# Kernel optimization log

Measured on AMD Instinct MI355X. Metric: run time of the kernel, lower is better.

Reference implementation:

```python
import jax, jax.numpy as jnp
import numpy as np

B, T, H, OUT = 128, 1024, 256, 2


def setup_inputs() -> dict:
    key = jax.random.key(0)
    ks = jax.random.split(key, 16)
    s_in = 1.0 / np.sqrt(1 + H)
    s_2h = 1.0 / np.sqrt(2 * H)
    s_o = 1.0 / np.sqrt(H)
    return {
        "x": jax.random.normal(ks[0], (B, T, 2), dtype=jnp.float32),
        "h_0": jax.random.normal(ks[1], (1, B, H), dtype=jnp.float32) * 0.1,
        "Wa": jax.random.normal(ks[2], (1 + H, H), dtype=jnp.float32) * s_in,
        "ba": jnp.zeros((H,), dtype=jnp.float32),
        "Wp1": jax.random.normal(ks[3], (1 + H, H), dtype=jnp.float32) * s_in,
        "bp1": jnp.zeros((H,), dtype=jnp.float32),
        "Wp2": jax.random.normal(ks[4], (1 + H, H), dtype=jnp.float32) * s_in,
        "bp2": jnp.zeros((H,), dtype=jnp.float32),
        "Wz": jax.random.normal(ks[5], (2 * H, H), dtype=jnp.float32) * s_2h,
        "bz": jnp.zeros((H,), dtype=jnp.float32),
        "Wh": jax.random.normal(ks[6], (2 * H, H), dtype=jnp.float32) * s_2h,
        "bh": jnp.zeros((H,), dtype=jnp.float32),
        "Wo": jax.random.normal(ks[7], (H, OUT), dtype=jnp.float32) * s_o,
        "bo": jnp.zeros((OUT,), dtype=jnp.float32),
    }


def _pgjanet_scan(x, h0, Wa, ba, Wp1, bp1, Wp2, bp2, Wz, bz, Wh, bh):
    # x: [B, T, 2], h0: [B, H]
    xt_all = jnp.swapaxes(x, 0, 1)  # [T, B, 2]

    def step(h, xt):
        amp = xt[:, 0:1]                       # [B, 1]
        ph = xt[:, 1:2]                        # [B, 1]
        a = jnp.tanh(jnp.concatenate([amp, h], axis=-1) @ Wa + ba)
        p1 = jnp.tanh(jnp.concatenate([jnp.cos(ph), h], axis=-1) @ Wp1 + bp1)
        p2 = jnp.tanh(jnp.concatenate([jnp.sin(ph), h], axis=-1) @ Wp2 + bp2)
        u = a * p1 * p2 * (1 - a) * (1 - p1) * (1 - p2)
        newin = jnp.concatenate([u, h], axis=-1)  # [B, 2H]
        z = jax.nn.sigmoid(newin @ Wz + bz)
        h_cand = jnp.tanh(newin @ Wh + bh)
        h_new = z * h + (1 - z) * h_cand
        return h_new, h_new

    h_n, hs = jax.lax.scan(step, h0, xt_all)
    return jnp.swapaxes(hs, 0, 1), h_n  # [B, T, H], [B, H]


def reference(x, h_0, Wa, ba, Wp1, bp1, Wp2, bp2, Wz, bz, Wh, bh, Wo, bo):
    hs, h_n = _pgjanet_scan(x, h_0[0], Wa, ba, Wp1, bp1, Wp2, bp2, Wz, bz, Wh, bh)
    out = hs @ Wo + bo  # [B, T, OUT]
    return (out, h_n)
```

## Files before the change

kernel.cpp:

```cpp
#include <hip/hip_runtime.h>
#include <math.h>


#define B_   128
#define T_   1024
#define H_   256
#define GB   16
#define GC   16
#define MB   8
#define NS   16
#define NTHR 512
#define HPAD 264

typedef float    f32x4 __attribute__((ext_vector_type(4)));
typedef unsigned u32x4 __attribute__((ext_vector_type(4)));

__device__ __forceinline__ void sys_st_x4(unsigned* p, u32x4 v) {
  asm volatile("global_store_dwordx4 %0, %1, off sc0 sc1" :: "v"(p), "v"(v) : "memory");
}
__device__ __forceinline__ void sys_ld2_x4(const unsigned* p0, const unsigned* p1,
                                           u32x4& a, u32x4& b) {
  asm volatile("global_load_dwordx4 %0, %2, off sc0 sc1\n\t"
               "global_load_dwordx4 %1, %3, off sc0 sc1\n\t"
               "s_waitcnt vmcnt(0)"
               : "=&v"(a), "=&v"(b) : "v"(p0), "v"(p1) : "memory");
}

__launch_bounds__(NTHR, 1)
__global__ void pgjanet_persist(
    const float* __restrict__ x,   const float* __restrict__ h0,
    const float* __restrict__ Wa,  const float* __restrict__ ba,
    const float* __restrict__ Wp1, const float* __restrict__ bp1,
    const float* __restrict__ Wp2, const float* __restrict__ bp2,
    const float* __restrict__ Wz,  const float* __restrict__ bz,
    const float* __restrict__ Wh,  const float* __restrict__ bh,
    const float* __restrict__ Wo,  const float* __restrict__ bo,
    float* __restrict__ out,
    unsigned* __restrict__ u_ex,
    unsigned* __restrict__ h_ex)
{
  __shared__ __align__(16) float w1t[3 * NS * 256];
  __shared__ __align__(16) float w2t[2 * NS * 512];
  __shared__ __align__(16) float h_lds[MB * HPAD];
  __shared__ __align__(16) float u_lds[MB * HPAD];
  __shared__ __align__(16) float wo_s[H_ * 2];
  __shared__ __align__(16) float xin[2 * MB * 4];

  const int wg   = blockIdx.x;
  const int g    = wg >> 4;
  const int gc   = wg & (GC - 1);
  const int tid  = threadIdx.x;
  const int lane = tid & 63;
  const int wave = tid >> 6;
  const int mb   = lane >> 3;
  const int ks   = lane & 7;
  const int b0   = g * MB;
  const int n0   = gc * NS + wave * 2;

  for (int i = tid; i < 3 * NS * 256; i += NTHR) {
    int c = i >> 8, k = i & 255;
    int mat = c >> 4, n = c & 15;
    const float* W = (mat == 0) ? Wa : (mat == 1 ? Wp1 : Wp2);
    w1t[i] = W[(1 + k) * H_ + gc * NS + n];
  }
  for (int i = tid; i < 2 * NS * 512; i += NTHR) {
    int c = i >> 9, k = i & 511;
    int mat = c >> 4, n = c & 15;
    const float* W = (mat == 0) ? Wz : Wh;
    w2t[i] = W[k * H_ + gc * NS + n];
  }
  for (int i = tid; i < H_ * 2; i += NTHR) wo_s[i] = Wo[i];

  float w1r0_[6], b1_[6];
#pragma unroll
  for (int m = 0; m < 3; ++m) {
    const float* W  = (m == 0) ? Wa : (m == 1 ? Wp1 : Wp2);
    const float* bb = (m == 0) ? ba : (m == 1 ? bp1 : bp2);
#pragma unroll
    for (int cc = 0; cc < 2; ++cc) {
      w1r0_[m * 2 + cc] = W[n0 + cc];
      b1_[m * 2 + cc]   = bb[n0 + cc];
    }
  }
  float bz_[2] = { bz[n0], bz[n0 + 1] };
  float bh_[2] = { bh[n0], bh[n0 + 1] };
  const float bo0 = bo[0], bo1 = bo[1];

  {
    int flat = tid * 4;
    int mbb = flat >> 8, kk = flat & 255;
    *(f32x4*)(h_lds + mbb * HPAD + kk) = *(const f32x4*)(h0 + (b0 + mbb) * H_ + kk);
  }
  if (tid < MB) {
    float2 xt = *(const float2*)(x + ((b0 + tid) * T_) * 2);
    f32x4 xi; xi[0] = xt.x; xi[1] = cosf(xt.y); xi[2] = sinf(xt.y); xi[3] = 0.f;
    *(f32x4*)(xin + tid * 4) = xi;
  }
  __syncthreads();

  unsigned* u_exg = u_ex + g * 4096;
  unsigned* h_exg = h_ex + g * 4096;
  unsigned* u_my  = u_exg + ((gc * 8 + wave) * 8) * 4;
  unsigned* h_my  = h_exg + ((gc * 8 + wave) * 8) * 4;

  for (int t = 0; t < T_; ++t) {
    const unsigned seq = (unsigned)(t + 1);

    f32x4 hv[8];
#pragma unroll
    for (int kt = 0; kt < 8; ++kt)
      hv[kt] = *(const f32x4*)(h_lds + mb * HPAD + kt * 32 + ks * 4);

    float acc[6] = {0.f, 0.f, 0.f, 0.f, 0.f, 0.f};
#pragma unroll
    for (int kt = 0; kt < 8; ++kt) {
      f32x4 h4 = hv[kt];
#pragma unroll
      for (int m = 0; m < 3; ++m)
#pragma unroll
        for (int cc = 0; cc < 2; ++cc) {
          f32x4 w4 = *(const f32x4*)(w1t + (m * NS + wave * 2 + cc) * 256 + kt * 32 + ks * 4);
          float s = acc[m * 2 + cc];
          s = fmaf(h4[0], w4[0], s); s = fmaf(h4[1], w4[1], s);
          s = fmaf(h4[2], w4[2], s); s = fmaf(h4[3], w4[3], s);
          acc[m * 2 + cc] = s;
        }
    }
#pragma unroll
    for (int i = 0; i < 6; ++i) {
      float v = acc[i];
      v += __shfl_xor(v, 1);
      v += __shfl_xor(v, 2);
      v += __shfl_xor(v, 4);
      acc[i] = v;
    }
    if (ks == 0) {
      f32x4 xi = *(const f32x4*)(xin + ((t & 1) * MB + mb) * 4);
      float uu[2];
#pragma unroll
      for (int cc = 0; cc < 2; ++cc) {
        float a  = tanhf(acc[0 + cc] + xi[0] * w1r0_[0 + cc] + b1_[0 + cc]);
        float p1 = tanhf(acc[2 + cc] + xi[1] * w1r0_[2 + cc] + b1_[2 + cc]);
        float p2 = tanhf(acc[4 + cc] + xi[2] * w1r0_[4 + cc] + b1_[4 + cc]);
        uu[cc] = a * p1 * p2 * (1.f - a) * (1.f - p1) * (1.f - p2);
      }
      u32x4 ch;
      ch.x = __float_as_uint(uu[0]); ch.y = __float_as_uint(uu[1]);
      ch.z = seq; ch.w = 0u;
      sys_st_x4(u_my + mb * 4, ch);
    }

    if (t + 1 < T_ && tid < MB) {
      float2 xt = *(const float2*)(x + ((b0 + tid) * T_ + (t + 1)) * 2);
      f32x4 xi; xi[0] = xt.x; xi[1] = cosf(xt.y); xi[2] = sinf(xt.y); xi[3] = 0.f;
      *(f32x4*)(xin + (((t + 1) & 1) * MB + tid) * 4) = xi;
    }
    if (t > 0 && ((t - 1) & 15) == gc) {
      f32x4 h4  = *(const f32x4*)(h_lds + wave * HPAD + lane * 4);
      f32x4 wo0 = *(const f32x4*)(wo_s + lane * 8);
      f32x4 wo1 = *(const f32x4*)(wo_s + lane * 8 + 4);
      float v0 = h4[0] * wo0[0] + h4[1] * wo0[2] + h4[2] * wo1[0] + h4[3] * wo1[2];
      float v1 = h4[0] * wo0[1] + h4[1] * wo0[3] + h4[2] * wo1[1] + h4[3] * wo1[3];
      v0 += __shfl_xor(v0, 1);  v1 += __shfl_xor(v1, 1);
      v0 += __shfl_xor(v0, 2);  v1 += __shfl_xor(v1, 2);
      v0 += __shfl_xor(v0, 4);  v1 += __shfl_xor(v1, 4);
      v0 += __shfl_xor(v0, 8);  v1 += __shfl_xor(v1, 8);
      v0 += __shfl_xor(v0, 16); v1 += __shfl_xor(v1, 16);
      v0 += __shfl_xor(v0, 32); v1 += __shfl_xor(v1, 32);
      if (lane == 0) {
        float2 o; o.x = v0 + bo0; o.y = v1 + bo1;
        *(float2*)(out + ((b0 + wave) * T_ + (t - 1)) * 2) = o;
      }
    }
    float acc2[4] = {0.f, 0.f, 0.f, 0.f};
#pragma unroll
    for (int kt = 0; kt < 8; ++kt) {
      f32x4 h4 = hv[kt];
#pragma unroll
      for (int m = 0; m < 2; ++m)
#pragma unroll
        for (int cc = 0; cc < 2; ++cc) {
          f32x4 w4 = *(const f32x4*)(w2t + (m * NS + wave * 2 + cc) * 512 + 256 + kt * 32 + ks * 4);
          float s = acc2[m * 2 + cc];
          s = fmaf(h4[0], w4[0], s); s = fmaf(h4[1], w4[1], s);
          s = fmaf(h4[2], w4[2], s); s = fmaf(h4[3], w4[3], s);
          acc2[m * 2 + cc] = s;
        }
    }

    {
      u32x4 A, B;
      const unsigned* p0 = u_exg + tid * 4;
      const unsigned* p1 = u_exg + (tid + 512) * 4;
      for (;;) {
        sys_ld2_x4(p0, p1, A, B);
        if (A.z == seq && B.z == seq) break;
        __builtin_amdgcn_s_sleep(1);
      }
      int c = tid;
      float2 d0; d0.x = __uint_as_float(A.x); d0.y = __uint_as_float(A.y);
      *(float2*)(u_lds + (c & 7) * HPAD + (c >> 6) * 16 + ((c >> 3) & 7) * 2) = d0;
      c = tid + 512;
      float2 d1; d1.x = __uint_as_float(B.x); d1.y = __uint_as_float(B.y);
      *(float2*)(u_lds + (c & 7) * HPAD + (c >> 6) * 16 + ((c >> 3) & 7) * 2) = d1;
    }
    __syncthreads();

#pragma unroll
    for (int kt = 0; kt < 8; ++kt) {
      f32x4 u4 = *(const f32x4*)(u_lds + mb * HPAD + kt * 32 + ks * 4);
#pragma unroll
      for (int m = 0; m < 2; ++m)
#pragma unroll
        for (int cc = 0; cc < 2; ++cc) {
          f32x4 w4 = *(const f32x4*)(w2t + (m * NS + wave * 2 + cc) * 512 + kt * 32 + ks * 4);
          float s = acc2[m * 2 + cc];
          s = fmaf(u4[0], w4[0], s); s = fmaf(u4[1], w4[1], s);
          s = fmaf(u4[2], w4[2], s); s = fmaf(u4[3], w4[3], s);
          acc2[m * 2 + cc] = s;
        }
    }
#pragma unroll
    for (int i = 0; i < 4; ++i) {
      float v = acc2[i];
      v += __shfl_xor(v, 1);
      v += __shfl_xor(v, 2);
      v += __shfl_xor(v, 4);
      acc2[i] = v;
    }
    if (ks == 0) {
      float z0  = 1.f / (1.f + expf(-(acc2[0] + bz_[0])));
      float z1  = 1.f / (1.f + expf(-(acc2[1] + bz_[1])));
      float hc0 = tanhf(acc2[2] + bh_[0]);
      float hc1 = tanhf(acc2[3] + bh_[1]);
      float2 hp = *(const float2*)(h_lds + mb * HPAD + n0);
      float hn0 = z0 * hp.x + (1.f - z0) * hc0;
      float hn1 = z1 * hp.y + (1.f - z1) * hc1;
      u32x4 ch;
      ch.x = __float_as_uint(hn0); ch.y = __float_as_uint(hn1);
      ch.z = seq; ch.w = 0u;
      sys_st_x4(h_my + mb * 4, ch);
      if (t == T_ - 1) {
        float2 o; o.x = hn0; o.y = hn1;
        *(float2*)(out + B_ * T_ * 2 + (b0 + mb) * H_ + n0) = o;
      }
    }
    __syncthreads();

    {
      u32x4 A, B;
      const unsigned* p0 = h_exg + tid * 4;
      const unsigned* p1 = h_exg + (tid + 512) * 4;
      for (;;) {
        sys_ld2_x4(p0, p1, A, B);
        if (A.z == seq && B.z == seq) break;
        __builtin_amdgcn_s_sleep(1);
      }
      int c = tid;
      float2 d0; d0.x = __uint_as_float(A.x); d0.y = __uint_as_float(A.y);
      *(float2*)(h_lds + (c & 7) * HPAD + (c >> 6) * 16 + ((c >> 3) & 7) * 2) = d0;
      c = tid + 512;
      float2 d1; d1.x = __uint_as_float(B.x); d1.y = __uint_as_float(B.y);
      *(float2*)(h_lds + (c & 7) * HPAD + (c >> 6) * 16 + ((c >> 3) & 7) * 2) = d1;
    }
    __syncthreads();
  }

  if (gc == ((T_ - 1) & 15)) {
    f32x4 h4  = *(const f32x4*)(h_lds + wave * HPAD + lane * 4);
    f32x4 wo0 = *(const f32x4*)(wo_s + lane * 8);
    f32x4 wo1 = *(const f32x4*)(wo_s + lane * 8 + 4);
    float v0 = h4[0] * wo0[0] + h4[1] * wo0[2] + h4[2] * wo1[0] + h4[3] * wo1[2];
    float v1 = h4[0] * wo0[1] + h4[1] * wo0[3] + h4[2] * wo1[1] + h4[3] * wo1[3];
    v0 += __shfl_xor(v0, 1);  v1 += __shfl_xor(v1, 1);
    v0 += __shfl_xor(v0, 2);  v1 += __shfl_xor(v1, 2);
    v0 += __shfl_xor(v0, 4);  v1 += __shfl_xor(v1, 4);
    v0 += __shfl_xor(v0, 8);  v1 += __shfl_xor(v1, 8);
    v0 += __shfl_xor(v0, 16); v1 += __shfl_xor(v1, 16);
    v0 += __shfl_xor(v0, 32); v1 += __shfl_xor(v1, 32);
    if (lane == 0) {
      float2 o; o.x = v0 + bo0; o.y = v1 + bo1;
      *(float2*)(out + ((b0 + wave) * T_ + (T_ - 1)) * 2) = o;
    }
  }
}

extern "C" void kernel_launch(void* const* d_in, const int* in_sizes, int n_in,
                              void* d_out, int out_size, void* d_ws, size_t ws_size,
                              hipStream_t stream) {
  (void)in_sizes; (void)n_in; (void)out_size; (void)ws_size;
  const float* x   = (const float*)d_in[0];
  const float* h0  = (const float*)d_in[1];
  const float* Wa  = (const float*)d_in[2];
  const float* ba  = (const float*)d_in[3];
  const float* Wp1 = (const float*)d_in[4];
  const float* bp1 = (const float*)d_in[5];
  const float* Wp2 = (const float*)d_in[6];
  const float* bp2 = (const float*)d_in[7];
  const float* Wz  = (const float*)d_in[8];
  const float* bz  = (const float*)d_in[9];
  const float* Wh  = (const float*)d_in[10];
  const float* bh  = (const float*)d_in[11];
  const float* Wo  = (const float*)d_in[12];
  const float* bo  = (const float*)d_in[13];

  float* out = (float*)d_out;
  char*  ws  = (char*)d_ws;
  unsigned* u_ex = (unsigned*)ws;
  unsigned* h_ex = (unsigned*)(ws + 262144);

  hipMemsetAsync(ws, 0, 524288, stream);

  pgjanet_persist<<<dim3(GB * GC), dim3(NTHR), 0, stream>>>(
      x, h0, Wa, ba, Wp1, bp1, Wp2, bp2, Wz, bz, Wh, bh, Wo, bo,
      out, u_ex, h_ex);
}
```

Before: 5.698 ms.

## Hold recurrent weights in registers with smaller batch groups and wider column slices

The work split changes from 16 column-groups by 8 batch rows to 8 column-groups by 4 batch rows, and each thread now keeps its slice of all five weight matrices in registers instead of reading them from LDS every step. Each 16-lane group computes one output column for all 4 batch rows, and the gate nonlinearities are spread across lanes with shuffles. Per-step exchange traffic drops to one poll load per thread. The cost is very high VGPR pressure (about 160 floats of weights per thread), more shuffle reductions, and fewer rows per group amortizing each cross-workgroup sync.

```diff
diff --git a/kernel.cpp b/kernel.cpp
--- a/kernel.cpp
+++ b/kernel.cpp
@@ -5,12 +5,12 @@
 #define B_   128
 #define T_   1024
 #define H_   256
-#define GB   16
-#define GC   16
-#define MB   8
-#define NS   16
+#define GB   32
+#define GC   8
+#define MB   4
+#define NS   32
 #define NTHR 512
-#define HPAD 264
+#define HP   260
 
 typedef float    f32x4 __attribute__((ext_vector_type(4)));
 typedef unsigned u32x4 __attribute__((ext_vector_type(4)));
@@ -18,12 +18,11 @@
 __device__ __forceinline__ void sys_st_x4(unsigned* p, u32x4 v) {
   asm volatile("global_store_dwordx4 %0, %1, off sc0 sc1" :: "v"(p), "v"(v) : "memory");
 }
-__device__ __forceinline__ void sys_ld2_x4(const unsigned* p0, const unsigned* p1,
-                                           u32x4& a, u32x4& b) {
-  asm volatile("global_load_dwordx4 %0, %2, off sc0 sc1\n\t"
-               "global_load_dwordx4 %1, %3, off sc0 sc1\n\t"
-               "s_waitcnt vmcnt(0)"
-               : "=&v"(a), "=&v"(b) : "v"(p0), "v"(p1) : "memory");
+__device__ __forceinline__ u32x4 sys_ld_x4(const unsigned* p) {
+  u32x4 v;
+  asm volatile("global_load_dwordx4 %0, %1, off sc0 sc1\n\ts_waitcnt vmcnt(0)"
+               : "=v"(v) : "v"(p) : "memory");
+  return v;
 }
 
 __launch_bounds__(NTHR, 1)
@@ -39,126 +38,201 @@
     unsigned* __restrict__ u_ex,
     unsigned* __restrict__ h_ex)
 {
-  __shared__ __align__(16) float w1t[3 * NS * 256];
-  __shared__ __align__(16) float w2t[2 * NS * 512];
-  __shared__ __align__(16) float h_lds[MB * HPAD];
-  __shared__ __align__(16) float u_lds[MB * HPAD];
+  __shared__ __align__(16) float h_lds[MB][HP];
+  __shared__ __align__(16) float u_lds[MB][HP];
   __shared__ __align__(16) float wo_s[H_ * 2];
-  __shared__ __align__(16) float xin[2 * MB * 4];
+  __shared__ __align__(16) float xin[2][MB][4];
 
   const int wg   = blockIdx.x;
-  const int g    = wg >> 4;
-  const int gc   = wg & (GC - 1);
+  const int g    = wg >> 3;
+  const int gc   = wg & 7;
   const int tid  = threadIdx.x;
-  const int lane = tid & 63;
-  const int wave = tid >> 6;
-  const int mb   = lane >> 3;
-  const int ks   = lane & 7;
+  const int col  = tid >> 4;
+  const int kk   = tid & 15;
   const int b0   = g * MB;
-  const int n0   = gc * NS + wave * 2;
-
-  for (int i = tid; i < 3 * NS * 256; i += NTHR) {
-    int c = i >> 8, k = i & 255;
-    int mat = c >> 4, n = c & 15;
-    const float* W = (mat == 0) ? Wa : (mat == 1 ? Wp1 : Wp2);
-    w1t[i] = W[(1 + k) * H_ + gc * NS + n];
-  }
-  for (int i = tid; i < 2 * NS * 512; i += NTHR) {
-    int c = i >> 9, k = i & 511;
-    int mat = c >> 4, n = c & 15;
-    const float* W = (mat == 0) ? Wz : Wh;
-    w2t[i] = W[k * H_ + gc * NS + n];
-  }
-  for (int i = tid; i < H_ * 2; i += NTHR) wo_s[i] = Wo[i];
-
-  float w1r0_[6], b1_[6];
+  const int colg = gc * NS + col;
+
+  f32x4 w1r[3][4]; float w1r0_[3], b1_[3];
 #pragma unroll
   for (int m = 0; m < 3; ++m) {
     const float* W  = (m == 0) ? Wa : (m == 1 ? Wp1 : Wp2);
     const float* bb = (m == 0) ? ba : (m == 1 ? bp1 : bp2);
 #pragma unroll
-    for (int cc = 0; cc < 2; ++cc) {
-      w1r0_[m * 2 + cc] = W[n0 + cc];
-      b1_[m * 2 + cc]   = bb[n0 + cc];
-    }
-  }
-  float bz_[2] = { bz[n0], bz[n0 + 1] };
-  float bh_[2] = { bh[n0], bh[n0 + 1] };
+    for (int j = 0; j < 4; ++j) {
+      f32x4 w;
+#pragma unroll
+      for (int c = 0; c < 4; ++c)
+        w[c] = W[(1 + kk * 4 + j * 64 + c) * H_ + colg];
+      w1r[m][j] = w;
+    }
+    w1r0_[m] = W[colg];
+    b1_[m]   = bb[colg];
+  }
+  f32x4 w2r[2][8];
+#pragma unroll
+  for (int m = 0; m < 2; ++m) {
+    const float* W = (m == 0) ? Wz : Wh;
+#pragma unroll
+    for (int j = 0; j < 8; ++j) {
+      int rb = (j < 4) ? (kk * 4 + j * 64) : (256 + kk * 4 + (j - 4) * 64);
+      f32x4 w;
+#pragma unroll
+      for (int c = 0; c < 4; ++c)
+        w[c] = W[(rb + c) * H_ + colg];
+      w2r[m][j] = w;
+    }
+  }
+  const float bz_c = bz[colg], bh_c = bh[colg];
   const float bo0 = bo[0], bo1 = bo[1];
-
+  for (int i = tid; i < H_ * 2; i += NTHR) wo_s[i] = Wo[i];
   {
-    int flat = tid * 4;
-    int mbb = flat >> 8, kk = flat & 255;
-    *(f32x4*)(h_lds + mbb * HPAD + kk) = *(const f32x4*)(h0 + (b0 + mbb) * H_ + kk);
+    int b = tid >> 7, c2 = (tid & 127) * 2;
+    float2 hv = *(const float2*)(h0 + (size_t)(b0 + b) * H_ + c2);
+    h_lds[b][c2] = hv.x; h_lds[b][c2 + 1] = hv.y;
   }
   if (tid < MB) {
-    float2 xt = *(const float2*)(x + ((b0 + tid) * T_) * 2);
-    f32x4 xi; xi[0] = xt.x; xi[1] = cosf(xt.y); xi[2] = sinf(xt.y); xi[3] = 0.f;
-    *(f32x4*)(xin + tid * 4) = xi;
+    float2 xt = *(const float2*)(x + ((size_t)(b0 + tid) * T_) * 2);
+    xin[0][tid][0] = xt.x; xin[0][tid][1] = cosf(xt.y);
+    xin[0][tid][2] = sinf(xt.y); xin[0][tid][3] = 0.f;
   }
   __syncthreads();
 
-  unsigned* u_exg = u_ex + g * 4096;
-  unsigned* h_exg = h_ex + g * 4096;
-  unsigned* u_my  = u_exg + ((gc * 8 + wave) * 8) * 4;
-  unsigned* h_my  = h_exg + ((gc * 8 + wave) * 8) * 4;
+  unsigned* u_exg = u_ex + g * 2048;
+  unsigned* h_exg = h_ex + g * 2048;
+  unsigned* u_my  = u_exg + (gc * 64 + (col >> 1) * 4) * 4;
+  unsigned* h_my  = h_exg + (gc * 64 + (col >> 1) * 4) * 4;
+  const unsigned* pu = u_exg + tid * 4;
+  const unsigned* ph = h_exg + tid * 4;
+  const int cpg = ((tid >> 6) * 16 + ((tid >> 2) & 15)) * 2;
+  const int cb  = tid & 3;
+  const int em  = kk >> 2, eb = kk & 3;
 
   for (int t = 0; t < T_; ++t) {
     const unsigned seq = (unsigned)(t + 1);
-
-    f32x4 hv[8];
-#pragma unroll
-    for (int kt = 0; kt < 8; ++kt)
-      hv[kt] = *(const f32x4*)(h_lds + mb * HPAD + kt * 32 + ks * 4);
-
-    float acc[6] = {0.f, 0.f, 0.f, 0.f, 0.f, 0.f};
-#pragma unroll
-    for (int kt = 0; kt < 8; ++kt) {
-      f32x4 h4 = hv[kt];
-#pragma unroll
-      for (int m = 0; m < 3; ++m)
-#pragma unroll
-        for (int cc = 0; cc < 2; ++cc) {
-          f32x4 w4 = *(const f32x4*)(w1t + (m * NS + wave * 2 + cc) * 256 + kt * 32 + ks * 4);
-          float s = acc[m * 2 + cc];
-          s = fmaf(h4[0], w4[0], s); s = fmaf(h4[1], w4[1], s);
-          s = fmaf(h4[2], w4[2], s); s = fmaf(h4[3], w4[3], s);
-          acc[m * 2 + cc] = s;
+    const int xb = t & 1;
+
+    float acc[12];
+#pragma unroll
+    for (int i = 0; i < 12; ++i) acc[i] = 0.f;
+#pragma unroll
+    for (int b = 0; b < MB; ++b) {
+#pragma unroll
+      for (int j = 0; j < 4; ++j) {
+        f32x4 h4 = *(const f32x4*)&h_lds[b][kk * 4 + j * 64];
+#pragma unroll
+        for (int m = 0; m < 3; ++m) {
+          float s = acc[m * 4 + b];
+          s = fmaf(h4[0], w1r[m][j][0], s); s = fmaf(h4[1], w1r[m][j][1], s);
+          s = fmaf(h4[2], w1r[m][j][2], s); s = fmaf(h4[3], w1r[m][j][3], s);
+          acc[m * 4 + b] = s;
         }
-    }
-#pragma unroll
-    for (int i = 0; i < 6; ++i) {
+      }
+    }
+#pragma unroll
+    for (int i = 0; i < 12; ++i) {
       float v = acc[i];
-      v += __shfl_xor(v, 1);
-      v += __shfl_xor(v, 2);
-      v += __shfl_xor(v, 4);
+      v += __shfl_xor(v, 1); v += __shfl_xor(v, 2);
+      v += __shfl_xor(v, 4); v += __shfl_xor(v, 8);
       acc[i] = v;
     }
-    if (ks == 0) {
-      f32x4 xi = *(const f32x4*)(xin + ((t & 1) * MB + mb) * 4);
-      float uu[2];
-#pragma unroll
-      for (int cc = 0; cc < 2; ++cc) {
-        float a  = tanhf(acc[0 + cc] + xi[0] * w1r0_[0 + cc] + b1_[0 + cc]);
-        float p1 = tanhf(acc[2 + cc] + xi[1] * w1r0_[2 + cc] + b1_[2 + cc]);
-        float p2 = tanhf(acc[4 + cc] + xi[2] * w1r0_[4 + cc] + b1_[4 + cc]);
-        uu[cc] = a * p1 * p2 * (1.f - a) * (1.f - p1) * (1.f - p2);
-      }
-      u32x4 ch;
-      ch.x = __float_as_uint(uu[0]); ch.y = __float_as_uint(uu[1]);
-      ch.z = seq; ch.w = 0u;
-      sys_st_x4(u_my + mb * 4, ch);
-    }
-
-    if (t + 1 < T_ && tid < MB) {
-      float2 xt = *(const float2*)(x + ((b0 + tid) * T_ + (t + 1)) * 2);
-      f32x4 xi; xi[0] = xt.x; xi[1] = cosf(xt.y); xi[2] = sinf(xt.y); xi[3] = 0.f;
-      *(f32x4*)(xin + (((t + 1) & 1) * MB + tid) * 4) = xi;
-    }
-    if (t > 0 && ((t - 1) & 15) == gc) {
-      f32x4 h4  = *(const f32x4*)(h_lds + wave * HPAD + lane * 4);
-      f32x4 wo0 = *(const f32x4*)(wo_s + lane * 8);
-      f32x4 wo1 = *(const f32x4*)(wo_s + lane * 8 + 4);
+    {
+      float pre1 = acc[0];
+#pragma unroll
+      for (int i = 1; i < 12; ++i) if (kk == i) pre1 = acc[i];
+      float w0  = em == 0 ? w1r0_[0] : (em == 1 ? w1r0_[1] : w1r0_[2]);
+      float bb1 = em == 0 ? b1_[0]   : (em == 1 ? b1_[1]   : b1_[2]);
+      f32x4 xi4 = *(const f32x4*)&xin[xb][eb][0];
+      float xim = em == 0 ? xi4[0] : (em == 1 ? xi4[1] : xi4[2]);
+      float tv  = tanhf(pre1 + xim * w0 + bb1);
+      float p1v = __shfl(tv, kk + 4, 16);
+      float p2v = __shfl(tv, kk + 8, 16);
+      float uv  = tv * p1v * p2v * (1.f - tv) * (1.f - p1v) * (1.f - p2v);
+      float uodd = __shfl_xor(uv, 16);
+      if (kk < 4 && !(col & 1)) {
+        u32x4 ch;
+        ch.x = __float_as_uint(uv); ch.y = __float_as_uint(uodd);
+        ch.z = seq; ch.w = 0u;
+        sys_st_x4(u_my + eb * 4, ch);
+      }
+    }
+
+    float acc2[8];
+#pragma unroll
+    for (int i = 0; i < 8; ++i) acc2[i] = 0.f;
+#pragma unroll
+    for (int b = 0; b < MB; ++b) {
+#pragma unroll
+      for (int j = 0; j < 4; ++j) {
+        f32x4 h4 = *(const f32x4*)&h_lds[b][kk * 4 + j * 64];
+#pragma unroll
+        for (int m = 0; m < 2; ++m) {
+          float s = acc2[m * 4 + b];
+          s = fmaf(h4[0], w2r[m][4 + j][0], s); s = fmaf(h4[1], w2r[m][4 + j][1], s);
+          s = fmaf(h4[2], w2r[m][4 + j][2], s); s = fmaf(h4[3], w2r[m][4 + j][3], s);
+          acc2[m * 4 + b] = s;
+        }
+      }
+    }
+
+    {
+      u32x4 c;
+      for (;;) {
+        c = sys_ld_x4(pu);
+        if (c.z == seq) break;
+        __builtin_amdgcn_s_sleep(1);
+      }
+      float2 d; d.x = __uint_as_float(c.x); d.y = __uint_as_float(c.y);
+      *(float2*)&u_lds[cb][cpg] = d;
+    }
+    __syncthreads();
+
+#pragma unroll
+    for (int b = 0; b < MB; ++b) {
+#pragma unroll
+      for (int j = 0; j < 4; ++j) {
+        f32x4 u4 = *(const f32x4*)&u_lds[b][kk * 4 + j * 64];
+#pragma unroll
+        for (int m = 0; m < 2; ++m) {
+          float s = acc2[m * 4 + b];
+          s = fmaf(u4[0], w2r[m][j][0], s); s = fmaf(u4[1], w2r[m][j][1], s);
+          s = fmaf(u4[2], w2r[m][j][2], s); s = fmaf(u4[3], w2r[m][j][3], s);
+          acc2[m * 4 + b] = s;
+        }
+      }
+    }
+#pragma unroll
+    for (int i = 0; i < 8; ++i) {
+      float v = acc2[i];
+      v += __shfl_xor(v, 1); v += __shfl_xor(v, 2);
+      v += __shfl_xor(v, 4); v += __shfl_xor(v, 8);
+      acc2[i] = v;
+    }
+    {
+      float pre2 = acc2[0];
+#pragma unroll
+      for (int i = 1; i < 8; ++i) if (kk == i) pre2 = acc2[i];
+      float v2 = pre2 + (em == 0 ? bz_c : bh_c);
+      float gv;
+      if (em == 0) gv = 1.f / (1.f + expf(-v2));
+      else         gv = tanhf(v2);
+      float hcv   = __shfl(gv, kk + 4, 16);
+      float hprev = h_lds[eb][colg];
+      float hn    = gv * hprev + (1.f - gv) * hcv;
+      float hnodd = __shfl_xor(hn, 16);
+      if (kk < 4 && !(col & 1)) {
+        u32x4 ch;
+        ch.x = __float_as_uint(hn); ch.y = __float_as_uint(hnodd);
+        ch.z = seq; ch.w = 0u;
+        sys_st_x4(h_my + eb * 4, ch);
+      }
+      if (t == T_ - 1 && kk < 4)
+        out[(size_t)B_ * T_ * 2 + (size_t)(b0 + eb) * H_ + colg] = hn;
+    }
+
+    if (t > 0 && gc < MB && tid < 64) {
+      f32x4 h4  = *(const f32x4*)&h_lds[gc][tid * 4];
+      f32x4 wo0 = *(const f32x4*)&wo_s[tid * 8];
+      f32x4 wo1 = *(const f32x4*)&wo_s[tid * 8 + 4];
       float v0 = h4[0] * wo0[0] + h4[1] * wo0[2] + h4[2] * wo1[0] + h4[3] * wo1[2];
       float v1 = h4[0] * wo0[1] + h4[1] * wo0[3] + h4[2] * wo1[1] + h4[3] * wo1[3];
       v0 += __shfl_xor(v0, 1);  v1 += __shfl_xor(v1, 1);
@@ -167,109 +241,35 @@
       v0 += __shfl_xor(v0, 8);  v1 += __shfl_xor(v1, 8);
       v0 += __shfl_xor(v0, 16); v1 += __shfl_xor(v1, 16);
       v0 += __shfl_xor(v0, 32); v1 += __shfl_xor(v1, 32);
-      if (lane == 0) {
+      if (tid == 0) {
         float2 o; o.x = v0 + bo0; o.y = v1 + bo1;
-        *(float2*)(out + ((b0 + wave) * T_ + (t - 1)) * 2) = o;
-      }
-    }
-    float acc2[4] = {0.f, 0.f, 0.f, 0.f};
-#pragma unroll
-    for (int kt = 0; kt < 8; ++kt) {
-      f32x4 h4 = hv[kt];
-#pragma unroll
-      for (int m = 0; m < 2; ++m)
-#pragma unroll
-        for (int cc = 0; cc < 2; ++cc) {
-          f32x4 w4 = *(const f32x4*)(w2t + (m * NS + wave * 2 + cc) * 512 + 256 + kt * 32 + ks * 4);
-          float s = acc2[m * 2 + cc];
-          s = fmaf(h4[0], w4[0], s); s = fmaf(h4[1], w4[1], s);
-          s = fmaf(h4[2], w4[2], s); s = fmaf(h4[3], w4[3], s);
-          acc2[m * 2 + cc] = s;
-        }
-    }
+        *(float2*)(out + ((size_t)(b0 + gc) * T_ + (t - 1)) * 2) = o;
+      }
+    }
+    if (t + 1 < T_ && tid < MB) {
+      float2 xt = *(const float2*)(x + ((size_t)(b0 + tid) * T_ + (t + 1)) * 2);
+      xin[xb ^ 1][tid][0] = xt.x; xin[xb ^ 1][tid][1] = cosf(xt.y);
+      xin[xb ^ 1][tid][2] = sinf(xt.y); xin[xb ^ 1][tid][3] = 0.f;
+    }
+    __syncthreads();
 
     {
-      u32x4 A, B;
-      const unsigned* p0 = u_exg + tid * 4;
-      const unsigned* p1 = u_exg + (tid + 512) * 4;
+      u32x4 c;
       for (;;) {
-        sys_ld2_x4(p0, p1, A, B);
-        if (A.z == seq && B.z == seq) break;
+        c = sys_ld_x4(ph);
+        if (c.z == seq) break;
         __builtin_amdgcn_s_sleep(1);
       }
-      int c = tid;
-      float2 d0; d0.x = __uint_as_float(A.x); d0.y = __uint_as_float(A.y);
-      *(float2*)(u_lds + (c & 7) * HPAD + (c >> 6) * 16 + ((c >> 3) & 7) * 2) = d0;
-      c = tid + 512;
-      float2 d1; d1.x = __uint_as_float(B.x); d1.y = __uint_as_float(B.y);
-      *(float2*)(u_lds + (c & 7) * HPAD + (c >> 6) * 16 + ((c >> 3) & 7) * 2) = d1;
+      float2 d; d.x = __uint_as_float(c.x); d.y = __uint_as_float(c.y);
+      *(float2*)&h_lds[cb][cpg] = d;
     }
     __syncthreads();
-
-#pragma unroll
-    for (int kt = 0; kt < 8; ++kt) {
-      f32x4 u4 = *(const f32x4*)(u_lds + mb * HPAD + kt * 32 + ks * 4);
-#pragma unroll
-      for (int m = 0; m < 2; ++m)
-#pragma unroll
-        for (int cc = 0; cc < 2; ++cc) {
-          f32x4 w4 = *(const f32x4*)(w2t + (m * NS + wave * 2 + cc) * 512 + kt * 32 + ks * 4);
-          float s = acc2[m * 2 + cc];
-          s = fmaf(u4[0], w4[0], s); s = fmaf(u4[1], w4[1], s);
-          s = fmaf(u4[2], w4[2], s); s = fmaf(u4[3], w4[3], s);
-          acc2[m * 2 + cc] = s;
-        }
-    }
-#pragma unroll
-    for (int i = 0; i < 4; ++i) {
-      float v = acc2[i];
-      v += __shfl_xor(v, 1);
-      v += __shfl_xor(v, 2);
-      v += __shfl_xor(v, 4);
-      acc2[i] = v;
-    }
-    if (ks == 0) {
-      float z0  = 1.f / (1.f + expf(-(acc2[0] + bz_[0])));
-      float z1  = 1.f / (1.f + expf(-(acc2[1] + bz_[1])));
-      float hc0 = tanhf(acc2[2] + bh_[0]);
-      float hc1 = tanhf(acc2[3] + bh_[1]);
-      float2 hp = *(const float2*)(h_lds + mb * HPAD + n0);
-      float hn0 = z0 * hp.x + (1.f - z0) * hc0;
-      float hn1 = z1 * hp.y + (1.f - z1) * hc1;
-      u32x4 ch;
-      ch.x = __float_as_uint(hn0); ch.y = __float_as_uint(hn1);
-      ch.z = seq; ch.w = 0u;
-      sys_st_x4(h_my + mb * 4, ch);
-      if (t == T_ - 1) {
-        float2 o; o.x = hn0; o.y = hn1;
-        *(float2*)(out + B_ * T_ * 2 + (b0 + mb) * H_ + n0) = o;
-      }
-    }
-    __syncthreads();
-
-    {
-      u32x4 A, B;
-      const unsigned* p0 = h_exg + tid * 4;
-      const unsigned* p1 = h_exg + (tid + 512) * 4;
-      for (;;) {
-        sys_ld2_x4(p0, p1, A, B);
-        if (A.z == seq && B.z == seq) break;
-        __builtin_amdgcn_s_sleep(1);
-      }
-      int c = tid;
-      float2 d0; d0.x = __uint_as_float(A.x); d0.y = __uint_as_float(A.y);
-      *(float2*)(h_lds + (c & 7) * HPAD + (c >> 6) * 16 + ((c >> 3) & 7) * 2) = d0;
-      c = tid + 512;
-      float2 d1; d1.x = __uint_as_float(B.x); d1.y = __uint_as_float(B.y);
-      *(float2*)(h_lds + (c & 7) * HPAD + (c >> 6) * 16 + ((c >> 3) & 7) * 2) = d1;
-    }
-    __syncthreads();
-  }
-
-  if (gc == ((T_ - 1) & 15)) {
-    f32x4 h4  = *(const f32x4*)(h_lds + wave * HPAD + lane * 4);
-    f32x4 wo0 = *(const f32x4*)(wo_s + lane * 8);
-    f32x4 wo1 = *(const f32x4*)(wo_s + lane * 8 + 4);
+  }
+
+  if (gc < MB && tid < 64) {
+    f32x4 h4  = *(const f32x4*)&h_lds[gc][tid * 4];
+    f32x4 wo0 = *(const f32x4*)&wo_s[tid * 8];
+    f32x4 wo1 = *(const f32x4*)&wo_s[tid * 8 + 4];
     float v0 = h4[0] * wo0[0] + h4[1] * wo0[2] + h4[2] * wo1[0] + h4[3] * wo1[2];
     float v1 = h4[0] * wo0[1] + h4[1] * wo0[3] + h4[2] * wo1[1] + h4[3] * wo1[3];
     v0 += __shfl_xor(v0, 1);  v1 += __shfl_xor(v1, 1);
@@ -278,9 +278,9 @@
     v0 += __shfl_xor(v0, 8);  v1 += __shfl_xor(v1, 8);
     v0 += __shfl_xor(v0, 16); v1 += __shfl_xor(v1, 16);
     v0 += __shfl_xor(v0, 32); v1 += __shfl_xor(v1, 32);
-    if (lane == 0) {
+    if (tid == 0) {
       float2 o; o.x = v0 + bo0; o.y = v1 + bo1;
-      *(float2*)(out + ((b0 + wave) * T_ + (T_ - 1)) * 2) = o;
+      *(float2*)(out + ((size_t)(b0 + gc) * T_ + (T_ - 1)) * 2) = o;
     }
   }
 }
```

New measurement: 6.948 ms. +21.9%, slower.
